# Optimization experiments

Measured on AMD Instinct MI355X. Metric: run time of the kernel, lower is better.

The kernel has to match this reference:

```python
import jax, jax.numpy as jnp
import numpy as np

ALPHA = 0.2  # LeakyReLU negative slope
NEG_INF = -9e15


def setup_inputs() -> dict:
    key = jax.random.key(0)
    k1, k2, k3, k4 = jax.random.split(key, 4)
    B, N, F_in, F_out = 8, 2048, 512, 256
    h = jax.random.normal(k1, (B, N, F_in), dtype=jnp.float32)
    adj = jax.random.randint(k2, (B, N, N), 0, 2, dtype=jnp.int32)
    W = jax.random.normal(k3, (F_in, F_out), dtype=jnp.float32) * (1.414 / np.sqrt(F_in))
    a = jax.random.normal(k4, (2 * F_out, 1), dtype=jnp.float32) * (1.414 / np.sqrt(2 * F_out))
    return {"h": h, "adj": adj, "W": W, "a": a}


def reference(h, adj, W, a):
    # Wh: [B, N, F_out]
    Wh = jnp.matmul(h, W)
    F_out = W.shape[1]
    a1 = a[:F_out, 0]   # [F_out] -> source (row i) part
    a2 = a[F_out:, 0]   # [F_out] -> target (col j) part
    # e[b,i,j] = leakyrelu(Wh[b,i]@a1 + Wh[b,j]@a2)  (decomposed concat-attention)
    f1 = jnp.einsum('bnf,f->bn', Wh, a1)  # [B, N]
    f2 = jnp.einsum('bnf,f->bn', Wh, a2)  # [B, N]
    e = f1[:, :, None] + f2[:, None, :]   # [B, N, N]
    e = jnp.where(e > 0, e, ALPHA * e)    # LeakyReLU
    e = jnp.where(adj > 0, e, NEG_INF)
    attention = jax.nn.softmax(e, axis=2)
    # dropout p=0.0 / eval mode: identity
    h_prime = jnp.matmul(attention, Wh)   # [B, N, F_out]
    return jax.nn.elu(h_prime)            # concat=True branch
```

## Files before the change

### kernel.cpp

```cpp
#include <hip/hip_runtime.h>
#include <hip/hip_bf16.h>

#define GAT_ALPHA 0.2f

typedef short bf16x8 __attribute__((ext_vector_type(8)));
typedef float f32x4 __attribute__((ext_vector_type(4)));

__device__ __forceinline__ unsigned f2bf_u(float x) {
  union { float f; unsigned u; } v; v.f = x;
  return (v.u + 0x7fffu + ((v.u >> 16) & 1u)) >> 16;
}
__device__ __forceinline__ unsigned short f2bf(float x) { return (unsigned short)f2bf_u(x); }

__global__ void k_wt(const float* __restrict__ W, unsigned short* __restrict__ WT) {
  int kb = blockIdx.x * 8;
  int f = threadIdx.x;
  bf16x8 o;
#pragma unroll
  for (int i = 0; i < 8; ++i) o[i] = (short)f2bf(W[(kb + i) * 256 + f]);
  *reinterpret_cast<bf16x8*>(WT + f * 512 + kb) = o;
}

__global__ __launch_bounds__(256) void k_pack(const int* __restrict__ adj,
                                              unsigned char* __restrict__ bm) {
  __shared__ unsigned char sb[2048];
  const int bId = blockIdx.x, t = threadIdx.x;
  const int4* base = reinterpret_cast<const int4*>(adj + (size_t)bId * 8 * 2048);
#pragma unroll
  for (int i = 0; i < 8; ++i) {
    int4 v0 = base[i * 512 + t * 2];
    int4 v1 = base[i * 512 + t * 2 + 1];
    unsigned by = (v0.x != 0)        | ((v0.y != 0) << 1) | ((v0.z != 0) << 2) |
                  ((v0.w != 0) << 3) | ((v1.x != 0) << 4) | ((v1.y != 0) << 5) |
                  ((v1.z != 0) << 6) | ((v1.w != 0) << 7);
    sb[i * 256 + (t & 15) * 16 + (t >> 4)] = (unsigned char)by;
  }
  __syncthreads();
  reinterpret_cast<uint2*>(bm + (size_t)bId * 2048)[t] =
      reinterpret_cast<const uint2*>(sb)[t];
}

__global__ __launch_bounds__(256, 4) void k_gemm1(
    const float* __restrict__ h, const unsigned short* __restrict__ WT,
    const float* __restrict__ avec,
    unsigned short* __restrict__ WhT,
    float* __restrict__ E1p, float* __restrict__ E1n,
    float* __restrict__ E2p, float* __restrict__ E2n)
{
  const int bx = blockIdx.x;
  const int b = bx & 7, ng = bx >> 3;
  const int n0 = ng * 16;
  const int t = threadIdx.x;
  const int lane = t & 63, w = t >> 6;
  const int l15 = lane & 15, q = lane >> 4;

  __shared__ __align__(16) unsigned short Wt[256 * 24];
  __shared__ float f1a[16], f2a[16];
  if (t < 16) { f1a[t] = 0.f; f2a[t] = 0.f; }

  f32x4 acc[4];
#pragma unroll
  for (int i = 0; i < 4; ++i) acc[i] = (f32x4){0.f, 0.f, 0.f, 0.f};

  const unsigned short* wtb = WT + (w * 64 + l15) * 512 + q * 8;
  const float* hrow = h + ((size_t)(b * 2048 + n0 + l15)) * 512 + q * 8;

  float4 hS0[2], hS1[2], hS2[2];
  hS0[0] = *reinterpret_cast<const float4*>(hrow);
  hS0[1] = *reinterpret_cast<const float4*>(hrow + 4);
  hS1[0] = *reinterpret_cast<const float4*>(hrow + 32);
  hS1[1] = *reinterpret_cast<const float4*>(hrow + 36);
  hS2[0] = *reinterpret_cast<const float4*>(hrow + 64);
  hS2[1] = *reinterpret_cast<const float4*>(hrow + 68);

#pragma unroll
  for (int k = 0; k < 16; ++k) {
    bf16x8 af[4];
#pragma unroll
    for (int mt = 0; mt < 4; ++mt)
      af[mt] = *reinterpret_cast<const bf16x8*>(wtb + mt * 16 * 512 + k * 32);
    float4 hN[2];
    if (k < 13) {
      hN[0] = *reinterpret_cast<const float4*>(hrow + (k + 3) * 32);
      hN[1] = *reinterpret_cast<const float4*>(hrow + (k + 3) * 32 + 4);
    }
    bf16x8 bb;
    {
      float4 x0 = hS0[0], x1 = hS0[1];
      bb[0] = (short)f2bf(x0.x); bb[1] = (short)f2bf(x0.y);
      bb[2] = (short)f2bf(x0.z); bb[3] = (short)f2bf(x0.w);
      bb[4] = (short)f2bf(x1.x); bb[5] = (short)f2bf(x1.y);
      bb[6] = (short)f2bf(x1.z); bb[7] = (short)f2bf(x1.w);
    }
#pragma unroll
    for (int mt = 0; mt < 4; ++mt)
      acc[mt] = __builtin_amdgcn_mfma_f32_16x16x32_bf16(af[mt], bb, acc[mt], 0, 0, 0);
    hS0[0] = hS1[0]; hS0[1] = hS1[1];
    hS1[0] = hS2[0]; hS1[1] = hS2[1];
    if (k < 13) { hS2[0] = hN[0]; hS2[1] = hN[1]; }
  }

  float s1 = 0.f, s2 = 0.f;
#pragma unroll
  for (int mt = 0; mt < 4; ++mt) {
#pragma unroll
    for (int r = 0; r < 4; ++r) {
      int f = w * 64 + mt * 16 + q * 4 + r;
      float v = acc[mt][r];
      Wt[f * 24 + l15] = f2bf(v);
      s1 += v * avec[f];
      s2 += v * avec[256 + f];
    }
  }
  s1 += __shfl_xor(s1, 16); s1 += __shfl_xor(s1, 32);
  s2 += __shfl_xor(s2, 16); s2 += __shfl_xor(s2, 32);
  __syncthreads();
  if (q == 0) {
    atomicAdd(&f1a[l15], s1);
    atomicAdd(&f2a[l15], s2);
  }
  {
    uint4 va = *reinterpret_cast<const uint4*>(Wt + t * 24);
    uint4 vb = *reinterpret_cast<const uint4*>(Wt + t * 24 + 8);
    unsigned short* dst = WhT + (size_t)(b * 256 + t) * 2048 + n0;
    *reinterpret_cast<uint4*>(dst) = va;
    *reinterpret_cast<uint4*>(dst + 8) = vb;
  }
  __syncthreads();
  if (t < 16) {
    int n = b * 2048 + n0 + t;
    float f1 = f1a[t], f2 = f2a[t];
    E1p[n] = __expf(f1);
    E1n[n] = __expf(GAT_ALPHA * f1);
    E2p[n] = __expf(f2);
    E2n[n] = __expf(GAT_ALPHA * f2);
  }
}

__device__ __forceinline__ void build_frag(
    unsigned short* dst, unsigned by, float e1p, float e1n,
    float4 epl, float4 eph, float4 enl, float4 enh, float& den)
{
  float p0 = (by & 1u)   ? fmaxf(e1p * epl.x, e1n * enl.x) : 0.f;
  float p1 = (by & 2u)   ? fmaxf(e1p * epl.y, e1n * enl.y) : 0.f;
  float p2 = (by & 4u)   ? fmaxf(e1p * epl.z, e1n * enl.z) : 0.f;
  float p3 = (by & 8u)   ? fmaxf(e1p * epl.w, e1n * enl.w) : 0.f;
  float p4 = (by & 16u)  ? fmaxf(e1p * eph.x, e1n * enh.x) : 0.f;
  float p5 = (by & 32u)  ? fmaxf(e1p * eph.y, e1n * enh.y) : 0.f;
  float p6 = (by & 64u)  ? fmaxf(e1p * eph.z, e1n * enh.z) : 0.f;
  float p7 = (by & 128u) ? fmaxf(e1p * eph.w, e1n * enh.w) : 0.f;
  den += ((p0 + p1) + (p2 + p3)) + ((p4 + p5) + (p6 + p7));
  uint4 pk;
  pk.x = f2bf_u(p0) | (f2bf_u(p1) << 16);
  pk.y = f2bf_u(p2) | (f2bf_u(p3) << 16);
  pk.z = f2bf_u(p4) | (f2bf_u(p5) << 16);
  pk.w = f2bf_u(p6) | (f2bf_u(p7) << 16);
  *reinterpret_cast<uint4*>(dst) = pk;
}

__global__ __launch_bounds__(512, 4) void k_gat(
    const unsigned char* __restrict__ bm, const unsigned short* __restrict__ WhT,
    const float* __restrict__ E1p, const float* __restrict__ E1n,
    const float* __restrict__ E2p, const float* __restrict__ E2n,
    float* __restrict__ out)
{
  const int bx = blockIdx.x;
  const int b = bx & 7, ig = bx >> 3;
  const int i0 = ig * 64;
  const int t = threadIdx.x;
  const int lane = t & 63, w = t >> 6;
  const int l15 = lane & 15, q = lane >> 4;
  const int m = t & 15, qk = (t >> 4) & 3, pp = t >> 6;
  const int rt0 = pp >> 2, ks = pp & 3;
  const int r0 = rt0 * 16 + m, r1 = r0 + 32;
  const int cb = ks * 32 + qk * 8;
  const int K = ks * 4 + qk;

  __shared__ __align__(16) unsigned short Pb[2][8192];
  __shared__ float den_l[64];
  if (t < 64) den_l[t] = 0.f;

  const float e1p0 = E1p[b * 2048 + i0 + r0], e1n0 = E1n[b * 2048 + i0 + r0];
  const float e1p1 = E1p[b * 2048 + i0 + r1], e1n1 = E1n[b * 2048 + i0 + r1];
  float d0 = 0.f, d1 = 0.f;

  f32x4 acc[4][2];
#pragma unroll
  for (int i = 0; i < 4; ++i)
#pragma unroll
    for (int j = 0; j < 2; ++j) acc[i][j] = (f32x4){0.f, 0.f, 0.f, 0.f};

  const unsigned char* bm0 = bm + ((size_t)(b * 2048 + i0 + r0)) * 256 + K * 16;
  const unsigned char* bm1 = bm0 + (size_t)32 * 256;
  const int e2b = b * 2048 + cb;
  const unsigned short* Wb = WhT + (size_t)(b * 256 + w * 32) * 2048;

  {
    unsigned by0 = bm0[0], by1 = bm1[0];
    float4 epl = *reinterpret_cast<const float4*>(E2p + e2b);
    float4 eph = *reinterpret_cast<const float4*>(E2p + e2b + 4);
    float4 enl = *reinterpret_cast<const float4*>(E2n + e2b);
    float4 enh = *reinterpret_cast<const float4*>(E2n + e2b + 4);
    build_frag(&Pb[0][(pp * 64 + lane) * 8], by0, e1p0, e1n0, epl, eph, enl, enh, d0);
    build_frag(&Pb[0][((pp + 8) * 64 + lane) * 8], by1, e1p1, e1n1, epl, eph, enl, enh, d1);
  }
  __syncthreads();

#pragma unroll 2
  for (int c = 0; c < 16; ++c) {
    bf16x8 bcur[2][4];
#pragma unroll
    for (int ct = 0; ct < 2; ++ct)
#pragma unroll
      for (int k2 = 0; k2 < 4; ++k2)
        bcur[ct][k2] = *reinterpret_cast<const bf16x8*>(
            Wb + (size_t)(ct * 16 + l15) * 2048 + c * 128 + k2 * 32 + q * 8);
    unsigned nby0 = 0, nby1 = 0;
    float4 nEpl, nEph, nEnl, nEnh;
    if (c < 15) {
      nby0 = bm0[c + 1];
      nby1 = bm1[c + 1];
      int o = (c + 1) * 128;
      nEpl = *reinterpret_cast<const float4*>(E2p + e2b + o);
      nEph = *reinterpret_cast<const float4*>(E2p + e2b + o + 4);
      nEnl = *reinterpret_cast<const float4*>(E2n + e2b + o);
      nEnh = *reinterpret_cast<const float4*>(E2n + e2b + o + 4);
    }
    const unsigned short* pb = &Pb[c & 1][0];
#pragma unroll
    for (int k2 = 0; k2 < 4; ++k2) {
      bf16x8 afr[4];
#pragma unroll
      for (int rt = 0; rt < 4; ++rt)
        afr[rt] = *reinterpret_cast<const bf16x8*>(pb + ((rt * 4 + k2) * 64 + lane) * 8);
#pragma unroll
      for (int rt = 0; rt < 4; ++rt)
#pragma unroll
        for (int ct = 0; ct < 2; ++ct)
          acc[rt][ct] = __builtin_amdgcn_mfma_f32_16x16x32_bf16(afr[rt], bcur[ct][k2], acc[rt][ct], 0, 0, 0);
    }
    if (c < 15) {
      unsigned short* wb = &Pb[(c + 1) & 1][0];
      build_frag(wb + (pp * 64 + lane) * 8, nby0, e1p0, e1n0, nEpl, nEph, nEnl, nEnh, d0);
      build_frag(wb + ((pp + 8) * 64 + lane) * 8, nby1, e1p1, e1n1, nEpl, nEph, nEnl, nEnh, d1);
      __syncthreads();
    }
  }

  d0 += __shfl_xor(d0, 16); d0 += __shfl_xor(d0, 32);
  d1 += __shfl_xor(d1, 16); d1 += __shfl_xor(d1, 32);
  if (lane < 16) {
    atomicAdd(&den_l[r0], d0);
    atomicAdd(&den_l[r1], d1);
  }
  __syncthreads();

#pragma unroll
  for (int rt = 0; rt < 4; ++rt) {
#pragma unroll
    for (int r = 0; r < 4; ++r) {
      int row = rt * 16 + q * 4 + r;
      float dinv = 1.0f / den_l[row];
      size_t ob = ((size_t)(b * 2048 + i0 + row)) * 256 + w * 32;
#pragma unroll
      for (int ct = 0; ct < 2; ++ct) {
        float v = acc[rt][ct][r] * dinv;
        v = v > 0.f ? v : (__expf(v) - 1.f);
        out[ob + ct * 16 + l15] = v;
      }
    }
  }
}

extern "C" void kernel_launch(void* const* d_in, const int* in_sizes, int n_in,
                              void* d_out, int out_size, void* d_ws, size_t ws_size,
                              hipStream_t stream) {
  const float* h   = (const float*)d_in[0];
  const int*   adj = (const int*)d_in[1];
  const float* W   = (const float*)d_in[2];
  const float* a   = (const float*)d_in[3];
  float* out = (float*)d_out;

  char* ws = (char*)d_ws;
  unsigned short* WhT = (unsigned short*)ws;
  unsigned short* WT  = (unsigned short*)(ws + 8388608);
  float* E1p = (float*)(ws + 8388608 + 262144);
  float* E1n = E1p + 16384;
  float* E2p = E1n + 16384;
  float* E2n = E2p + 16384;
  unsigned char* bm = (unsigned char*)(ws + 8388608 + 262144 + 4 * 65536);

  k_wt<<<dim3(64), dim3(256), 0, stream>>>(W, WT);
  k_pack<<<dim3(2048), dim3(256), 0, stream>>>(adj, bm);
  k_gemm1<<<dim3(1024), dim3(256), 0, stream>>>(h, WT, a, WhT, E1p, E1n, E2p, E2n);
  k_gat<<<dim3(256), dim3(512), 0, stream>>>(bm, WhT, E1p, E1n, E2p, E2n, out);
}
```

Before: 315.6 us.

## Build attention fragments in registers and split GAT kernel over feature groups

The attention kernel no longer stages probability fragments in double-buffered shared memory with barriers. Each wave now builds its A-fragment in registers directly from a repacked adjacency bitmask, whose byte order in the pack kernel is changed to match. The row-sum denominator comes from an extra MFMA against a ones vector instead of shuffles and LDS atomics. The grid grows to 1024 blocks of 256 threads, each covering 64 rows by 64 features, with register prefetch of the next Wh tile. In exchange, every feature-group block recomputes the exp/mask fragments, four times the elementwise work.

Result: slower. 406.1 us (+28.7%).

```diff
diff --git a/kernel.cpp b/kernel.cpp
--- a/kernel.cpp
+++ b/kernel.cpp
@@ -33,7 +33,7 @@
     unsigned by = (v0.x != 0)        | ((v0.y != 0) << 1) | ((v0.z != 0) << 2) |
                   ((v0.w != 0) << 3) | ((v1.x != 0) << 4) | ((v1.y != 0) << 5) |
                   ((v1.z != 0) << 6) | ((v1.w != 0) << 7);
-    sb[i * 256 + (t & 15) * 16 + (t >> 4)] = (unsigned char)by;
+    sb[i * 256 + (t & 3) * 64 + (t >> 2)] = (unsigned char)by;
   }
   __syncthreads();
   reinterpret_cast<uint2*>(bm + (size_t)bId * 2048)[t] =
@@ -137,9 +137,9 @@
   }
 }
 
-__device__ __forceinline__ void build_frag(
-    unsigned short* dst, unsigned by, float e1p, float e1n,
-    float4 epl, float4 eph, float4 enl, float4 enh, float& den)
+__device__ __forceinline__ bf16x8 build_frag_r(
+    unsigned by, float e1p, float e1n,
+    float4 epl, float4 eph, float4 enl, float4 enh)
 {
   float p0 = (by & 1u)   ? fmaxf(e1p * epl.x, e1n * enl.x) : 0.f;
   float p1 = (by & 2u)   ? fmaxf(e1p * epl.y, e1n * enl.y) : 0.f;
@@ -149,125 +149,94 @@
   float p5 = (by & 32u)  ? fmaxf(e1p * eph.y, e1n * enh.y) : 0.f;
   float p6 = (by & 64u)  ? fmaxf(e1p * eph.z, e1n * enh.z) : 0.f;
   float p7 = (by & 128u) ? fmaxf(e1p * eph.w, e1n * enh.w) : 0.f;
-  den += ((p0 + p1) + (p2 + p3)) + ((p4 + p5) + (p6 + p7));
-  uint4 pk;
-  pk.x = f2bf_u(p0) | (f2bf_u(p1) << 16);
-  pk.y = f2bf_u(p2) | (f2bf_u(p3) << 16);
-  pk.z = f2bf_u(p4) | (f2bf_u(p5) << 16);
-  pk.w = f2bf_u(p6) | (f2bf_u(p7) << 16);
-  *reinterpret_cast<uint4*>(dst) = pk;
-}
-
-__global__ __launch_bounds__(512, 4) void k_gat(
+  union { unsigned u[4]; bf16x8 v; } pk;
+  pk.u[0] = f2bf_u(p0) | (f2bf_u(p1) << 16);
+  pk.u[1] = f2bf_u(p2) | (f2bf_u(p3) << 16);
+  pk.u[2] = f2bf_u(p4) | (f2bf_u(p5) << 16);
+  pk.u[3] = f2bf_u(p6) | (f2bf_u(p7) << 16);
+  return pk.v;
+}
+
+__global__ __launch_bounds__(256, 4) void k_gat(
     const unsigned char* __restrict__ bm, const unsigned short* __restrict__ WhT,
     const float* __restrict__ E1p, const float* __restrict__ E1n,
     const float* __restrict__ E2p, const float* __restrict__ E2n,
     float* __restrict__ out)
 {
   const int bx = blockIdx.x;
-  const int b = bx & 7, ig = bx >> 3;
-  const int i0 = ig * 64;
+  const int b = bx & 7, fg = (bx >> 3) & 3, rg = bx >> 5;
+  const int i0 = rg * 64, f0 = fg * 64;
   const int t = threadIdx.x;
   const int lane = t & 63, w = t >> 6;
-  const int l15 = lane & 15, q = lane >> 4;
-  const int m = t & 15, qk = (t >> 4) & 3, pp = t >> 6;
-  const int rt0 = pp >> 2, ks = pp & 3;
-  const int r0 = rt0 * 16 + m, r1 = r0 + 32;
-  const int cb = ks * 32 + qk * 8;
-  const int K = ks * 4 + qk;
-
-  __shared__ __align__(16) unsigned short Pb[2][8192];
-  __shared__ float den_l[64];
-  if (t < 64) den_l[t] = 0.f;
-
-  const float e1p0 = E1p[b * 2048 + i0 + r0], e1n0 = E1n[b * 2048 + i0 + r0];
-  const float e1p1 = E1p[b * 2048 + i0 + r1], e1n1 = E1n[b * 2048 + i0 + r1];
-  float d0 = 0.f, d1 = 0.f;
-
-  f32x4 acc[4][2];
-#pragma unroll
-  for (int i = 0; i < 4; ++i)
-#pragma unroll
-    for (int j = 0; j < 2; ++j) acc[i][j] = (f32x4){0.f, 0.f, 0.f, 0.f};
-
-  const unsigned char* bm0 = bm + ((size_t)(b * 2048 + i0 + r0)) * 256 + K * 16;
-  const unsigned char* bm1 = bm0 + (size_t)32 * 256;
-  const int e2b = b * 2048 + cb;
-  const unsigned short* Wb = WhT + (size_t)(b * 256 + w * 32) * 2048;
-
-  {
-    unsigned by0 = bm0[0], by1 = bm1[0];
-    float4 epl = *reinterpret_cast<const float4*>(E2p + e2b);
-    float4 eph = *reinterpret_cast<const float4*>(E2p + e2b + 4);
-    float4 enl = *reinterpret_cast<const float4*>(E2n + e2b);
-    float4 enh = *reinterpret_cast<const float4*>(E2n + e2b + 4);
-    build_frag(&Pb[0][(pp * 64 + lane) * 8], by0, e1p0, e1n0, epl, eph, enl, enh, d0);
-    build_frag(&Pb[0][((pp + 8) * 64 + lane) * 8], by1, e1p1, e1n1, epl, eph, enl, enh, d1);
-  }
-  __syncthreads();
-
-#pragma unroll 2
-  for (int c = 0; c < 16; ++c) {
-    bf16x8 bcur[2][4];
-#pragma unroll
-    for (int ct = 0; ct < 2; ++ct)
-#pragma unroll
-      for (int k2 = 0; k2 < 4; ++k2)
-        bcur[ct][k2] = *reinterpret_cast<const bf16x8*>(
-            Wb + (size_t)(ct * 16 + l15) * 2048 + c * 128 + k2 * 32 + q * 8);
-    unsigned nby0 = 0, nby1 = 0;
-    float4 nEpl, nEph, nEnl, nEnh;
-    if (c < 15) {
-      nby0 = bm0[c + 1];
-      nby1 = bm1[c + 1];
-      int o = (c + 1) * 128;
-      nEpl = *reinterpret_cast<const float4*>(E2p + e2b + o);
-      nEph = *reinterpret_cast<const float4*>(E2p + e2b + o + 4);
-      nEnl = *reinterpret_cast<const float4*>(E2n + e2b + o);
-      nEnh = *reinterpret_cast<const float4*>(E2n + e2b + o + 4);
-    }
-    const unsigned short* pb = &Pb[c & 1][0];
-#pragma unroll
-    for (int k2 = 0; k2 < 4; ++k2) {
-      bf16x8 afr[4];
-#pragma unroll
-      for (int rt = 0; rt < 4; ++rt)
-        afr[rt] = *reinterpret_cast<const bf16x8*>(pb + ((rt * 4 + k2) * 64 + lane) * 8);
-#pragma unroll
-      for (int rt = 0; rt < 4; ++rt)
-#pragma unroll
-        for (int ct = 0; ct < 2; ++ct)
-          acc[rt][ct] = __builtin_amdgcn_mfma_f32_16x16x32_bf16(afr[rt], bcur[ct][k2], acc[rt][ct], 0, 0, 0);
-    }
-    if (c < 15) {
-      unsigned short* wb = &Pb[(c + 1) & 1][0];
-      build_frag(wb + (pp * 64 + lane) * 8, nby0, e1p0, e1n0, nEpl, nEph, nEnl, nEnh, d0);
-      build_frag(wb + ((pp + 8) * 64 + lane) * 8, nby1, e1p1, e1n1, nEpl, nEph, nEnl, nEnh, d1);
-      __syncthreads();
-    }
-  }
-
-  d0 += __shfl_xor(d0, 16); d0 += __shfl_xor(d0, 32);
-  d1 += __shfl_xor(d1, 16); d1 += __shfl_xor(d1, 32);
-  if (lane < 16) {
-    atomicAdd(&den_l[r0], d0);
-    atomicAdd(&den_l[r1], d1);
-  }
-  __syncthreads();
-
-#pragma unroll
-  for (int rt = 0; rt < 4; ++rt) {
-#pragma unroll
-    for (int r = 0; r < 4; ++r) {
-      int row = rt * 16 + q * 4 + r;
-      float dinv = 1.0f / den_l[row];
-      size_t ob = ((size_t)(b * 2048 + i0 + row)) * 256 + w * 32;
-#pragma unroll
-      for (int ct = 0; ct < 2; ++ct) {
-        float v = acc[rt][ct][r] * dinv;
-        v = v > 0.f ? v : (__expf(v) - 1.f);
-        out[ob + ct * 16 + l15] = v;
+  const int m = lane & 15, q = lane >> 4;
+  const int row = i0 + w * 16 + m;
+
+  const unsigned char* bmr = bm + ((size_t)(b * 2048 + row)) * 256 + q * 64;
+  uint4 bmv0 = *reinterpret_cast<const uint4*>(bmr);
+  uint4 bmv1 = *reinterpret_cast<const uint4*>(bmr + 16);
+  uint4 bmv2 = *reinterpret_cast<const uint4*>(bmr + 32);
+  uint4 bmv3 = *reinterpret_cast<const uint4*>(bmr + 48);
+
+  const float e1p = E1p[b * 2048 + row], e1n = E1n[b * 2048 + row];
+  const int e2b = b * 2048 + q * 8;
+
+  f32x4 acc[4], accd;
+#pragma unroll
+  for (int i = 0; i < 4; ++i) acc[i] = (f32x4){0.f, 0.f, 0.f, 0.f};
+  accd = (f32x4){0.f, 0.f, 0.f, 0.f};
+
+  bf16x8 ones;
+#pragma unroll
+  for (int i = 0; i < 8; ++i) ones[i] = (short)0x3F80;
+
+  const unsigned short* Wb = WhT + (size_t)(b * 256 + f0) * 2048 + q * 8;
+
+  bf16x8 Bc[4], Bn[4];
+#pragma unroll
+  for (int ct = 0; ct < 4; ++ct)
+    Bc[ct] = *reinterpret_cast<const bf16x8*>(Wb + (size_t)(ct * 16 + m) * 2048);
+
+  for (int w4 = 0; w4 < 4; ++w4) {
+    uint4 bv = (w4 == 0) ? bmv0 : (w4 == 1) ? bmv1 : (w4 == 2) ? bmv2 : bmv3;
+#pragma unroll
+    for (int s2 = 0; s2 < 16; ++s2) {
+      const int s = w4 * 16 + s2;
+      unsigned bw = ((s2 >> 2) == 0) ? bv.x : ((s2 >> 2) == 1) ? bv.y
+                  : ((s2 >> 2) == 2) ? bv.z : bv.w;
+      unsigned by = (bw >> ((s2 & 3) * 8)) & 0xffu;
+      const float* p2p = E2p + e2b + s * 32;
+      const float* p2n = E2n + e2b + s * 32;
+      float4 epl = *reinterpret_cast<const float4*>(p2p);
+      float4 eph = *reinterpret_cast<const float4*>(p2p + 4);
+      float4 enl = *reinterpret_cast<const float4*>(p2n);
+      float4 enh = *reinterpret_cast<const float4*>(p2n + 4);
+      if (s < 63) {
+        const unsigned short* pB = Wb + (s + 1) * 32;
+#pragma unroll
+        for (int ct = 0; ct < 4; ++ct)
+          Bn[ct] = *reinterpret_cast<const bf16x8*>(pB + (size_t)(ct * 16 + m) * 2048);
       }
+      bf16x8 af = build_frag_r(by, e1p, e1n, epl, eph, enl, enh);
+#pragma unroll
+      for (int ct = 0; ct < 4; ++ct)
+        acc[ct] = __builtin_amdgcn_mfma_f32_16x16x32_bf16(af, Bc[ct], acc[ct], 0, 0, 0);
+      accd = __builtin_amdgcn_mfma_f32_16x16x32_bf16(af, ones, accd, 0, 0, 0);
+      if (s < 63) {
+#pragma unroll
+        for (int ct = 0; ct < 4; ++ct) Bc[ct] = Bn[ct];
+      }
+    }
+  }
+
+#pragma unroll
+  for (int r = 0; r < 4; ++r) {
+    float dinv = 1.0f / accd[r];
+    size_t ob = ((size_t)(b * 2048 + i0 + w * 16 + q * 4 + r)) * 256 + f0;
+#pragma unroll
+    for (int ct = 0; ct < 4; ++ct) {
+      float v = acc[ct][r] * dinv;
+      v = v > 0.f ? v : (__expf(v) - 1.f);
+      out[ob + ct * 16 + m] = v;
     }
   }
 }
@@ -293,5 +262,5 @@
   k_wt<<<dim3(64), dim3(256), 0, stream>>>(W, WT);
   k_pack<<<dim3(2048), dim3(256), 0, stream>>>(adj, bm);
   k_gemm1<<<dim3(1024), dim3(256), 0, stream>>>(h, WT, a, WhT, E1p, E1n, E2p, E2n);
-  k_gat<<<dim3(256), dim3(512), 0, stream>>>(bm, WhT, E1p, E1n, E2p, E2n, out);
-}
+  k_gat<<<dim3(1024), dim3(256), 0, stream>>>(bm, WhT, E1p, E1n, E2p, E2n, out);
+}
```
